# Kernel optimization log

Measured on AMD Instinct MI355X. Metric: run time of the kernel, lower is better.

Reference implementation:

```python
import jax, jax.numpy as jnp
import numpy as np

N_CLASSES = 256
GT_CLASSES = 21
DIM = 384
EPS = 1e-12  # matches torch F.normalize default eps


def setup_inputs() -> dict:
    key = jax.random.key(0)
    k1, k2, k3 = jax.random.split(key, 3)
    features = jax.random.normal(k1, (4, 256, 256, DIM), dtype=jnp.float32)
    weight = jax.random.uniform(k2, (4, 256, 256), dtype=jnp.float32)
    cluster_centers = jax.random.normal(k3, (N_CLASSES, DIM), dtype=jnp.float32)
    pseudo_assignment = (jnp.arange(N_CLASSES) % GT_CLASSES).astype(jnp.int32)
    return {
        "features": features,
        "weight": weight,
        "cluster_centers": cluster_centers,
        "pseudo_assignment": pseudo_assignment,
    }


def _l2norm(x, axis):
    # torch F.normalize: x / max(||x||, eps)
    n = jnp.sqrt(jnp.sum(x * x, axis=axis, keepdims=True))
    return x / jnp.maximum(n, EPS)


def reference(features, weight, cluster_centers, pseudo_assignment):
    lead_shape = features.shape[:-1]
    feats = features.reshape(-1, features.shape[-1])        # [N, D]
    w = weight.reshape(-1)                                   # [N]

    normed_clusters = _l2norm(cluster_centers, axis=1)       # [K, D]
    normed_features = _l2norm(feats, axis=1)                 # [N, D]

    inner_products = normed_features @ normed_clusters.T     # [N, K]
    class_labels = jnp.argmax(inner_products, axis=1)        # [N]

    # -(one_hot(labels) * inner_products).sum(1) == -inner_products[n, labels[n]]
    cluster_loss = -jnp.take_along_axis(
        inner_products, class_labels[:, None], axis=1
    )[:, 0]                                                  # [N]

    loss = jnp.mean(cluster_loss * w)

    pseudo_segs_pred = class_labels.reshape(lead_shape)
    segs_pred = pseudo_assignment[pseudo_segs_pred].astype(jnp.int64)
    return pseudo_segs_pred, segs_pred, loss
```

## Files before the change

kernel.cpp:

```cpp
#include <hip/hip_runtime.h>
#include <hip/hip_bf16.h>

#define NTOT (4*256*256)
#define DIM 384
#define KCL 256
#define BM 64
#define BK 32
#define TBS 256
#define GRID_MAIN (NTOT/BM)
#define NT (DIM/BK)
#define EPS 1e-12f

#define AH_OFF 0
#define AL_OFF 4096
#define BH_OFF 8192
#define BL_OFF 24576
#define BUF_BYTES 40960

typedef __attribute__((ext_vector_type(8))) _Float16 f16x8;
typedef __attribute__((ext_vector_type(4))) float f32x4;

__device__ __forceinline__ void async_copy16(const void* gptr, void* lptr) {
    __builtin_amdgcn_global_load_lds(
        (const __attribute__((address_space(1))) unsigned int*)gptr,
        (__attribute__((address_space(3))) unsigned int*)lptr, 16, 0, 0);
}

__global__ void prep_clusters(const float* __restrict__ cc,
                              _Float16* __restrict__ bh, _Float16* __restrict__ bl) {
    int j = blockIdx.x, l = threadIdx.x;
    float v[6]; float ssq = 0.f;
#pragma unroll
    for (int i = 0; i < 6; ++i) { v[i] = cc[j*DIM + l + 64*i]; ssq = fmaf(v[i], v[i], ssq); }
#pragma unroll
    for (int off = 32; off >= 1; off >>= 1) ssq += __shfl_xor(ssq, off);
    float inv = 1.f / fmaxf(sqrtf(ssq), EPS);
#pragma unroll
    for (int i = 0; i < 6; ++i) {
        float x = v[i] * inv;
        _Float16 h  = (_Float16)x;
        _Float16 lo = (_Float16)(x - (float)h);
        bh[j*DIM + l + 64*i] = h;
        bl[j*DIM + l + 64*i] = lo;
    }
}

__global__ __launch_bounds__(TBS, 4)
void kmeans_main(const float* __restrict__ A,
                 const float* __restrict__ W,
                 const _Float16* __restrict__ Bh,
                 const _Float16* __restrict__ Bl,
                 const int*   __restrict__ PA,
                 float* __restrict__ out,
                 float* __restrict__ partial)
{
    __shared__ unsigned char smem[BUF_BYTES];

    const int tid  = threadIdx.x;
    const int wv   = tid >> 6;
    const int lane = tid & 63;
    const int g    = lane >> 4;
    const int l15  = lane & 15;
    const int sw   = (l15 >> 1) & 3;
    const int row0 = blockIdx.x * BM;
    const int arow = tid >> 2, achk = tid & 3;
    const int bg   = (tid & 3) ^ ((tid >> 3) & 3);
    const int awb  = (((arow << 2) + (achk ^ ((arow >> 1) & 3))) << 4);
    const int fa   = l15 * 64 + ((g ^ sw) << 4);
    const int fb   = wv * 4096 + fa;

    const float* aptr = A + (size_t)(row0 + arow) * DIM + achk * 8;

    f32x4 acc[4][4];
#pragma unroll
    for (int m = 0; m < 4; ++m)
#pragma unroll
        for (int n = 0; n < 4; ++n) acc[m][n] = (f32x4){0.f, 0.f, 0.f, 0.f};
    float ssq = 0.f;

    auto stageB = [&](int ks) {
#pragma unroll
        for (int i = 0; i < 4; ++i) {
            int row = i * 64 + (tid >> 2);
            async_copy16(Bh + (size_t)row * DIM + ks + 8 * bg,
                         smem + BH_OFF + ((i * 256 + tid) << 4));
            async_copy16(Bl + (size_t)row * DIM + ks + 8 * bg,
                         smem + BL_OFF + ((i * 256 + tid) << 4));
        }
    };
    auto writeA = [&](const float4& x0, const float4& x1) {
        float av[8] = {x0.x, x0.y, x0.z, x0.w, x1.x, x1.y, x1.z, x1.w};
        f16x8 h8, l8;
#pragma unroll
        for (int w = 0; w < 8; ++w) {
            _Float16 hh = (_Float16)av[w];
            h8[w] = hh;
            l8[w] = (_Float16)(av[w] - (float)hh);
            ssq = fmaf(av[w], av[w], ssq);
        }
        *(f16x8*)(smem + AH_OFF + awb) = h8;
        *(f16x8*)(smem + AL_OFF + awb) = l8;
    };
    auto compute = [&]() {
        f16x8 ahf[4], alf[4], bhf[4], blf[4];
#pragma unroll
        for (int m = 0; m < 4; ++m) {
            ahf[m] = *(const f16x8*)(smem + AH_OFF + fa + m * 1024);
            alf[m] = *(const f16x8*)(smem + AL_OFF + fa + m * 1024);
        }
#pragma unroll
        for (int n = 0; n < 4; ++n) {
            bhf[n] = *(const f16x8*)(smem + BH_OFF + fb + n * 1024);
            blf[n] = *(const f16x8*)(smem + BL_OFF + fb + n * 1024);
        }
#pragma unroll
        for (int m = 0; m < 4; ++m)
#pragma unroll
            for (int n = 0; n < 4; ++n)
                acc[m][n] = __builtin_amdgcn_mfma_f32_16x16x32_f16(ahf[m], bhf[n], acc[m][n], 0, 0, 0);
#pragma unroll
        for (int m = 0; m < 4; ++m)
#pragma unroll
            for (int n = 0; n < 4; ++n)
                acc[m][n] = __builtin_amdgcn_mfma_f32_16x16x32_f16(ahf[m], blf[n], acc[m][n], 0, 0, 0);
#pragma unroll
        for (int m = 0; m < 4; ++m)
#pragma unroll
            for (int n = 0; n < 4; ++n)
                acc[m][n] = __builtin_amdgcn_mfma_f32_16x16x32_f16(alf[m], bhf[n], acc[m][n], 0, 0, 0);
    };

    {
        float4 c0 = *(const float4*)(aptr);
        float4 c1 = *(const float4*)(aptr + 4);
        stageB(0);
        writeA(c0, c1);
        __syncthreads();
    }

    for (int t = 0; t < NT - 1; ++t) {
        float4 n0 = *(const float4*)(aptr + (t + 1) * BK);
        float4 n1 = *(const float4*)(aptr + (t + 1) * BK + 4);
        compute();
        __syncthreads();
        stageB((t + 1) * BK);
        writeA(n0, n1);
        __syncthreads();
    }
    compute();
    __syncthreads();

    float* rowssq = (float*)smem;
    float* wvalp  = (float*)(smem + 256);
    int*   wcolp  = (int*)(smem + 1280);

    ssq += __shfl_xor(ssq, 1);
    ssq += __shfl_xor(ssq, 2);
    if (achk == 0) rowssq[arow] = ssq;

#pragma unroll
    for (int m = 0; m < 4; ++m) {
#pragma unroll
        for (int j = 0; j < 4; ++j) {
            float best = acc[m][0][j];
            int   bc   = wv * 64 + l15;
#pragma unroll
            for (int n = 1; n < 4; ++n) {
                float v = acc[m][n][j];
                int   c = wv * 64 + 16 * n + l15;
                if (v > best) { best = v; bc = c; }
            }
#pragma unroll
            for (int off = 1; off < 16; off <<= 1) {
                float ov = __shfl_xor(best, off);
                int   oc = __shfl_xor(bc, off);
                if (ov > best || (ov == best && oc < bc)) { best = ov; bc = oc; }
            }
            if (l15 == 0) {
                wvalp[wv * BM + 16 * m + 4 * g + j] = best;
                wcolp[wv * BM + 16 * m + 4 * g + j] = bc;
            }
        }
    }
    __syncthreads();

    if (tid < BM) {
        int r = tid;
        float best = wvalp[r]; int bc = wcolp[r];
#pragma unroll
        for (int w = 1; w < 4; ++w) {
            float ov = wvalp[w * BM + r]; int oc = wcolp[w * BM + r];
            if (ov > best || (ov == best && oc < bc)) { best = ov; bc = oc; }
        }
        float inv = 1.f / fmaxf(sqrtf(rowssq[r]), EPS);
        out[row0 + r]        = (float)bc;
        out[NTOT + row0 + r] = (float)PA[bc];
        float lsum = -(best * inv) * W[row0 + r];
#pragma unroll
        for (int off = 32; off >= 1; off >>= 1) lsum += __shfl_xor(lsum, off);
        if (tid == 0) partial[blockIdx.x] = lsum;
    }
}

__global__ void loss_reduce(const float* __restrict__ partial, float* __restrict__ out_loss) {
    __shared__ float s[256];
    float v = 0.f;
    for (int i = threadIdx.x; i < GRID_MAIN; i += 256) v += partial[i];
    s[threadIdx.x] = v;
    __syncthreads();
    for (int off = 128; off >= 1; off >>= 1) {
        if ((int)threadIdx.x < off) s[threadIdx.x] += s[threadIdx.x + off];
        __syncthreads();
    }
    if (threadIdx.x == 0) out_loss[0] = s[0] * (1.0f / (float)NTOT);
}

extern "C" void kernel_launch(void* const* d_in, const int* in_sizes, int n_in,
                              void* d_out, int out_size, void* d_ws, size_t ws_size,
                              hipStream_t stream) {
    const float* features = (const float*)d_in[0];
    const float* weight   = (const float*)d_in[1];
    const float* cc       = (const float*)d_in[2];
    const int*   pa       = (const int*)d_in[3];
    float* out = (float*)d_out;

    _Float16* bh = (_Float16*)d_ws;
    _Float16* bl = bh + KCL * DIM;
    float* partial = (float*)(bl + KCL * DIM);

    hipLaunchKernelGGL(prep_clusters, dim3(KCL), dim3(64), 0, stream, cc, bh, bl);
    hipLaunchKernelGGL(kmeans_main, dim3(GRID_MAIN), dim3(TBS), 0, stream,
                       features, weight, bh, bl, pa, out, partial);
    hipLaunchKernelGGL(loss_reduce, dim3(1), dim3(256), 0, stream, partial, out + 2 * NTOT);
}
```

Baseline: 211.0 us.

## Double-buffer A tiles, pre-swizzle cluster layout, and give each wave private B staging

Cluster centers are written in a tiled layout that matches the MFMA fragment order, so each wave can async-copy its own B slice into a private LDS region with contiguous, lane-linear loads. A tiles are double-buffered and the loop is unrolled by two with hand-placed waitcnt and s_barrier, plus s_setprio around the MFMA block, so global loads and LDS staging overlap compute. The aim is fewer full barriers and better load/compute overlap. In exchange LDS grows to 48KB and the occupancy hint drops to 3 blocks per CU, and the hand-written sync ordering is fragile.

```diff
diff --git a/kernel.cpp b/kernel.cpp
--- a/kernel.cpp
+++ b/kernel.cpp
@@ -11,11 +11,10 @@
 #define NT (DIM/BK)
 #define EPS 1e-12f
 
-#define AH_OFF 0
-#define AL_OFF 4096
-#define BH_OFF 8192
-#define BL_OFF 24576
-#define BUF_BYTES 40960
+#define ABUF(p)   ((p) * 8192)
+#define AHI 0
+#define ALO 4096
+#define BPRIV     16384
 
 typedef __attribute__((ext_vector_type(8))) _Float16 f16x8;
 typedef __attribute__((ext_vector_type(4))) float f32x4;
@@ -37,15 +36,18 @@
     float inv = 1.f / fmaxf(sqrtf(ssq), EPS);
 #pragma unroll
     for (int i = 0; i < 6; ++i) {
+        int d = l + 64 * i;
         float x = v[i] * inv;
         _Float16 h  = (_Float16)x;
         _Float16 lo = (_Float16)(x - (float)h);
-        bh[j*DIM + l + 64*i] = h;
-        bl[j*DIM + l + 64*i] = lo;
-    }
-}
-
-__global__ __launch_bounds__(TBS, 4)
+        size_t idx = (size_t)(((d >> 5) * 1024 + (j >> 4) * 64 + ((d >> 3) & 3) * 16 + (j & 15)) * 8
+                              + (d & 7));
+        bh[idx] = h;
+        bl[idx] = lo;
+    }
+}
+
+__global__ __launch_bounds__(TBS, 3)
 void kmeans_main(const float* __restrict__ A,
                  const float* __restrict__ W,
                  const _Float16* __restrict__ Bh,
@@ -54,7 +56,7 @@
                  float* __restrict__ out,
                  float* __restrict__ partial)
 {
-    __shared__ unsigned char smem[BUF_BYTES];
+    __shared__ unsigned char smem[49152];
 
     const int tid  = threadIdx.x;
     const int wv   = tid >> 6;
@@ -64,10 +66,12 @@
     const int sw   = (l15 >> 1) & 3;
     const int row0 = blockIdx.x * BM;
     const int arow = tid >> 2, achk = tid & 3;
-    const int bg   = (tid & 3) ^ ((tid >> 3) & 3);
     const int awb  = (((arow << 2) + (achk ^ ((arow >> 1) & 3))) << 4);
     const int fa   = l15 * 64 + ((g ^ sw) << 4);
-    const int fb   = wv * 4096 + fa;
+
+    const int bpb  = BPRIV + wv * 8192 + lane * 16;
+    const unsigned char* bhsrc = (const unsigned char*)Bh + (size_t)(4 * wv) * 1024 + lane * 16;
+    const unsigned char* blsrc = (const unsigned char*)Bl + (size_t)(4 * wv) * 1024 + lane * 16;
 
     const float* aptr = A + (size_t)(row0 + arow) * DIM + achk * 8;
 
@@ -78,17 +82,16 @@
         for (int n = 0; n < 4; ++n) acc[m][n] = (f32x4){0.f, 0.f, 0.f, 0.f};
     float ssq = 0.f;
 
-    auto stageB = [&](int ks) {
-#pragma unroll
-        for (int i = 0; i < 4; ++i) {
-            int row = i * 64 + (tid >> 2);
-            async_copy16(Bh + (size_t)row * DIM + ks + 8 * bg,
-                         smem + BH_OFF + ((i * 256 + tid) << 4));
-            async_copy16(Bl + (size_t)row * DIM + ks + 8 * bg,
-                         smem + BL_OFF + ((i * 256 + tid) << 4));
-        }
-    };
-    auto writeA = [&](const float4& x0, const float4& x1) {
+    auto stageB = [&](int t) {
+        const unsigned char* sh = bhsrc + (size_t)t * 16384;
+        const unsigned char* sl = blsrc + (size_t)t * 16384;
+#pragma unroll
+        for (int n = 0; n < 4; ++n) {
+            async_copy16(sh + n * 1024, smem + bpb + n * 1024);
+            async_copy16(sl + n * 1024, smem + bpb + 4096 + n * 1024);
+        }
+    };
+    auto writeA = [&](const float4& x0, const float4& x1, int q) {
         float av[8] = {x0.x, x0.y, x0.z, x0.w, x1.x, x1.y, x1.z, x1.w};
         f16x8 h8, l8;
 #pragma unroll
@@ -98,21 +101,27 @@
             l8[w] = (_Float16)(av[w] - (float)hh);
             ssq = fmaf(av[w], av[w], ssq);
         }
-        *(f16x8*)(smem + AH_OFF + awb) = h8;
-        *(f16x8*)(smem + AL_OFF + awb) = l8;
-    };
-    auto compute = [&]() {
-        f16x8 ahf[4], alf[4], bhf[4], blf[4];
+        *(f16x8*)(smem + ABUF(q) + AHI + awb) = h8;
+        *(f16x8*)(smem + ABUF(q) + ALO + awb) = l8;
+    };
+
+    f16x8 bhf[4], blf[4];
+    auto readB = [&]() {
+#pragma unroll
+        for (int n = 0; n < 4; ++n) {
+            bhf[n] = *(const f16x8*)(smem + bpb + n * 1024);
+            blf[n] = *(const f16x8*)(smem + bpb + 4096 + n * 1024);
+        }
+    };
+    auto mfmaBlock = [&](int p) {
+        f16x8 ahf[4], alf[4];
 #pragma unroll
         for (int m = 0; m < 4; ++m) {
-            ahf[m] = *(const f16x8*)(smem + AH_OFF + fa + m * 1024);
-            alf[m] = *(const f16x8*)(smem + AL_OFF + fa + m * 1024);
-        }
-#pragma unroll
-        for (int n = 0; n < 4; ++n) {
-            bhf[n] = *(const f16x8*)(smem + BH_OFF + fb + n * 1024);
-            blf[n] = *(const f16x8*)(smem + BL_OFF + fb + n * 1024);
-        }
+            ahf[m] = *(const f16x8*)(smem + ABUF(p) + AHI + fa + m * 1024);
+            alf[m] = *(const f16x8*)(smem + ABUF(p) + ALO + fa + m * 1024);
+        }
+        asm volatile("s_barrier" ::: "memory");
+        __builtin_amdgcn_s_setprio(1);
 #pragma unroll
         for (int m = 0; m < 4; ++m)
 #pragma unroll
@@ -128,26 +137,51 @@
 #pragma unroll
             for (int n = 0; n < 4; ++n)
                 acc[m][n] = __builtin_amdgcn_mfma_f32_16x16x32_f16(alf[m], bhf[n], acc[m][n], 0, 0, 0);
-    };
-
-    {
-        float4 c0 = *(const float4*)(aptr);
-        float4 c1 = *(const float4*)(aptr + 4);
-        stageB(0);
-        writeA(c0, c1);
-        __syncthreads();
-    }
-
-    for (int t = 0; t < NT - 1; ++t) {
-        float4 n0 = *(const float4*)(aptr + (t + 1) * BK);
-        float4 n1 = *(const float4*)(aptr + (t + 1) * BK + 4);
-        compute();
-        __syncthreads();
-        stageB((t + 1) * BK);
-        writeA(n0, n1);
-        __syncthreads();
-    }
-    compute();
+        __builtin_amdgcn_s_setprio(0);
+    };
+
+    float4 rA0x = *(const float4*)(aptr);
+    float4 rA0y = *(const float4*)(aptr + 4);
+    stageB(0);
+    float4 rA1x = *(const float4*)(aptr + BK);
+    float4 rA1y = *(const float4*)(aptr + BK + 4);
+    writeA(rA0x, rA0y, 0);
+    asm volatile("s_waitcnt lgkmcnt(0)" ::: "memory");
+    asm volatile("s_barrier" ::: "memory");
+
+    for (int t = 0; t < NT; t += 2) {
+        {
+            asm volatile("s_waitcnt vmcnt(0)" ::: "memory");
+            if (t + 2 < NT) {
+                rA0x = *(const float4*)(aptr + (t + 2) * BK);
+                rA0y = *(const float4*)(aptr + (t + 2) * BK + 4);
+            }
+            readB();
+            writeA(rA1x, rA1y, 1);
+            asm volatile("s_waitcnt lgkmcnt(0)" ::: "memory");
+            stageB(t + 1);
+            asm volatile("s_barrier" ::: "memory");
+            mfmaBlock(0);
+        }
+        {
+            const int tt = t + 1;
+            asm volatile("s_waitcnt vmcnt(0)" ::: "memory");
+            if (tt + 2 < NT) {
+                rA1x = *(const float4*)(aptr + (tt + 2) * BK);
+                rA1y = *(const float4*)(aptr + (tt + 2) * BK + 4);
+            }
+            readB();
+            if (tt + 1 < NT) {
+                writeA(rA0x, rA0y, 0);
+                asm volatile("s_waitcnt lgkmcnt(0)" ::: "memory");
+                stageB(tt + 1);
+            } else {
+                asm volatile("s_waitcnt lgkmcnt(0)" ::: "memory");
+            }
+            asm volatile("s_barrier" ::: "memory");
+            mfmaBlock(1);
+        }
+    }
     __syncthreads();
 
     float* rowssq = (float*)smem;
```

Measured after the change: 213.0 us. Within noise of the previous version (+1.0%).
